# Performance work log

Measured on AMD Instinct MI355X. Metric: run time of the kernel, lower is better.

## Reference

```python
import jax, jax.numpy as jnp
import numpy as np

B, N, HID = 1, 2048, 1024
H, WK, WV = 16, 64, 64
DH = HID // H  # 64


def setup_inputs() -> dict:
    key = jax.random.key(0)
    ks = jax.random.split(key, 10)
    s = 0.02
    return {
        "hidden_states": jax.random.normal(ks[0], (B, N, HID), jnp.float32),
        "attention_mask": jnp.ones((B, N), jnp.float32),
        "Wq": jax.random.normal(ks[1], (HID, HID), jnp.float32) * s,
        "bq": jnp.zeros((HID,), jnp.float32),
        "Wk": jax.random.normal(ks[2], (HID, HID), jnp.float32) * s,
        "bk": jnp.zeros((HID,), jnp.float32),
        "Wv": jax.random.normal(ks[3], (HID, HID), jnp.float32) * s,
        "bv": jnp.zeros((HID,), jnp.float32),
        # Conv1D(2*WK+1, DH, bias=False): weight [nx=DH, nf=2*WK+1]
        "W_rel_k": jax.random.normal(ks[4], (DH, 2 * WK + 1), jnp.float32) * s,
        # relative_pos_val: [2*WV+1, DH]
        "W_rel_v": jax.random.normal(ks[5], (2 * WV + 1, DH), jnp.float32) * s,
    }


def _attention(hidden_states, attention_mask, Wq, bq, Wk, bk, Wv, bv, W_rel_k, W_rel_v):
    b, n, _ = hidden_states.shape

    def heads(x):  # [B,N,HID] -> [B,H,N,DH]
        return x.reshape(b, n, H, DH).transpose(0, 2, 1, 3)

    q = heads(hidden_states @ Wq + bq)
    k = heads(hidden_states @ Wk + bk)
    v = heads(hidden_states @ Wv + bv)

    scores = jnp.einsum("bhid,bhjd->bhij", q, k)  # [B,H,N,N]

    # --- relative-position key bias: bias[i, j] = q_i . w_{j-i+WK} for |j-i|<=WK ---
    a_k = jnp.einsum("bhid,dw->bhiw", q, W_rel_k)  # [B,H,N,2*WK+1]
    rows = jnp.arange(n)
    slot = rows[None, :] - rows[:, None] + WK       # [N,N] relative slot j-i+WK
    valid_k = (slot >= 0) & (slot <= 2 * WK)
    bias = a_k[:, :, rows[:, None], jnp.clip(slot, 0, 2 * WK)]  # [B,H,N,N]
    scores = scores + jnp.where(valid_k, bias, 0.0)

    scores = scores / np.float32(np.sqrt(DH))  # temperature == 1.0

    # extended attention mask: (1 - mask) * dtype_min added to scores
    ext = (1.0 - attention_mask)[:, None, None, :] * jnp.finfo(scores.dtype).min
    scores = scores + ext

    probs = jax.nn.softmax(scores, axis=-1)  # [B,H,N,N]

    ctx = jnp.einsum("bhij,bhjd->bhid", probs, v)  # [B,H,N,DH]

    # --- relative-position value: band[i, r] = probs[i, i-WV+r]; ctx += band @ W_rel_v ---
    offs = jnp.arange(2 * WV + 1)
    kpos = rows[:, None] - WV + offs[None, :]       # [N, 2*WV+1] absolute key position
    valid_v = (kpos >= 0) & (kpos < n)
    band = probs[:, :, rows[:, None], jnp.clip(kpos, 0, n - 1)]  # [B,H,N,2*WV+1]
    band = jnp.where(valid_v, band, 0.0)
    ctx = ctx + jnp.einsum("bhiw,wd->bhid", band, W_rel_v)

    # merge heads -> [B,N,HID]
    return ctx.transpose(0, 2, 1, 3).reshape(b, n, HID)


def reference(hidden_states, attention_mask, Wq, bq, Wk, bk, Wv, bv, W_rel_k, W_rel_v):
    return _attention(hidden_states, attention_mask, Wq, bq, Wk, bk, Wv, bv, W_rel_k, W_rel_v)
```

## Files before the change

kernel.cpp:

```cpp
#include <hip/hip_runtime.h>
#include <hip/hip_bf16.h>

#define NSEQ 2048
#define HIDDIM 1024
#define NH 16
#define DHEAD 64
#define NW 129
#define AKS 132

typedef float          f32x4 __attribute__((ext_vector_type(4)));
typedef _Float16       f16x4 __attribute__((ext_vector_type(4)));
typedef _Float16       f16x8 __attribute__((ext_vector_type(8)));
typedef unsigned short u16;

__device__ __forceinline__ float b2f(u16 u){ return __uint_as_float(((unsigned)u) << 16); }
__device__ __forceinline__ float ld_any(const void* p, long idx, int flag){
  return flag ? b2f(((const u16*)p)[idx]) : ((const float*)p)[idx];
}

#define GLOAD_LDS16(gp, lp) \
  __builtin_amdgcn_global_load_lds((const __attribute__((address_space(1))) unsigned int*)(gp), \
                                   (__attribute__((address_space(3))) unsigned int*)(lp), 16, 0, 0)

static const size_t OFF_Q    = 0;
static const size_t OFF_K    = (size_t)4  << 20;
static const size_t OFF_VT   = (size_t)8  << 20;
static const size_t OFF_WT   = (size_t)12 << 20;
static const size_t OFF_AK   = (size_t)18 << 20;
static const size_t OFF_M    = OFF_AK + (size_t)NH * NSEQ * AKS * 4;
static const size_t OFF_L    = OFF_M + (size_t)2 * NH * NSEQ * 4;
static const size_t OFF_CTXP = OFF_L + (size_t)2 * NH * NSEQ * 4;
static const size_t OFF_HSF  = OFF_CTXP + (size_t)2 * NSEQ * HIDDIM * 4;
static const size_t OFF_BIAS = OFF_HSF + (size_t)NSEQ * HIDDIM * 2;
static const size_t OFF_WRK  = OFF_BIAS + 3 * 1024 * 4;
static const size_t OFF_WRV  = OFF_WRK + (size_t)DHEAD * NW * 4;
static const size_t OFF_EXT  = OFF_WRV + (size_t)NW * DHEAD * 4;
static const size_t OFF_FLAG = OFF_EXT + (size_t)NSEQ * 4;

__global__ void detect_kernel(const unsigned* __restrict__ mask_raw, int* __restrict__ flagp){
  *flagp = (mask_raw[0] == 0x3F800000u) ? 0 : 1;
}

__global__ void cvt_hs_kernel(const void* __restrict__ hs, const int* __restrict__ flagp,
                              _Float16* __restrict__ hsf){
  const int flag = *flagp;
  const long base = (long)(blockIdx.x * 256 + threadIdx.x) * 8;
  f16x8 o;
  if (flag){
    const u16* b = (const u16*)hs;
#pragma unroll
    for (int e = 0; e < 8; e++) o[e] = (_Float16)b2f(b[base + e]);
  } else {
    const float* f = (const float*)hs;
#pragma unroll
    for (int e = 0; e < 8; e++) o[e] = (_Float16)f[base + e];
  }
  *(f16x8*)(hsf + base) = o;
}

__global__ void cvt_small_kernel(const void* __restrict__ bq, const void* __restrict__ bk,
                                 const void* __restrict__ bv, const void* __restrict__ wrk,
                                 const void* __restrict__ wrv, const void* __restrict__ mask,
                                 const int* __restrict__ flagp,
                                 float* __restrict__ biasf, float* __restrict__ wrkf,
                                 float* __restrict__ wrvf, float* __restrict__ extf){
  const int flag = *flagp;
  const int idx = blockIdx.x * 256 + threadIdx.x;
  if (idx < 1024)            biasf[idx] = ld_any(bq, idx, flag);
  else if (idx < 2048)       biasf[idx] = ld_any(bk, idx - 1024, flag);
  else if (idx < 3072)       biasf[idx] = ld_any(bv, idx - 2048, flag);
  else if (idx < 3072 + 8256)  wrkf[idx - 3072]  = ld_any(wrk, idx - 3072, flag);
  else if (idx < 3072 + 16512) wrvf[idx - 11328] = ld_any(wrv, idx - 11328, flag);
  else if (idx < 3072 + 16512 + 2048)
    extf[idx - 19584] = (1.f - ld_any(mask, idx - 19584, flag)) * -1.0e30f;
}

__global__ void wtrans_kernel(const void* __restrict__ Wq, const void* __restrict__ Wk,
                              const void* __restrict__ Wv, const int* __restrict__ flagp,
                              _Float16* __restrict__ Wt){
  __shared__ __attribute__((aligned(16))) _Float16 tile[64][65];
  const int flag = *flagp;
  const int z = blockIdx.z;
  const void* src = (z == 0) ? Wq : ((z == 1) ? Wk : Wv);
  _Float16* dst = Wt + (size_t)z * 1024 * 1024;
  const int o0 = blockIdx.x * 64, k0 = blockIdx.y * 64;
  const int t = threadIdx.x;
#pragma unroll
  for (int c = 0; c < 2; c++){
    int idx = t + 256 * c;
    int r = idx >> 3, c8 = (idx & 7) * 8;
    long off = (long)(k0 + r) * 1024 + o0 + c8;
#pragma unroll
    for (int e = 0; e < 8; e++) tile[r][c8 + e] = (_Float16)ld_any(src, off + e, flag);
  }
  __syncthreads();
#pragma unroll
  for (int c = 0; c < 2; c++){
    int idx = t + 256 * c;
    int orow = idx >> 3, k8 = (idx & 7) * 8;
    f16x8 v;
#pragma unroll
    for (int e = 0; e < 8; e++) v[e] = tile[k8 + e][orow];
    *(f16x8*)(dst + (size_t)(o0 + orow) * 1024 + k0 + k8) = v;
  }
}

__launch_bounds__(256, 3)
__global__ void qkv_kernel(const _Float16* __restrict__ hsf, const _Float16* __restrict__ Wt,
                           const float* __restrict__ biasf,
                           _Float16* __restrict__ Qf, _Float16* __restrict__ Kf,
                           _Float16* __restrict__ Vtf){
  __shared__ __attribute__((aligned(16))) _Float16 As[2 * 64 * 32];
  __shared__ __attribute__((aligned(16))) _Float16 Bs[2 * 128 * 32];
  const int z = blockIdx.z;
  const _Float16* Wz = Wt + (size_t)z * 1024 * 1024;
  const int o0 = blockIdx.x * 128, m0 = blockIdx.y * 64;
  const int t = threadIdx.x, lane = t & 63, wave = t >> 6;
  const int wm = wave >> 1, wn = wave & 1;
  const int q = lane >> 4, ln = lane & 15;

  auto stage = [&](int nb, int k0){
    {
      const int row = t >> 2, chunk = t & 3;
      const _Float16* gA = hsf + (size_t)(m0 + row) * 1024 + k0 + chunk * 8;
      _Float16* lA = (_Float16*)As + nb * 2048 + (wave << 9);
      GLOAD_LDS16(gA, lA);
    }
#pragma unroll
    for (int p = 0; p < 2; p++){
      const int idx = p * 256 + t;
      const int row = idx >> 2, chunk = idx & 3;
      const _Float16* gB = Wz + (size_t)(o0 + row) * 1024 + k0 + chunk * 8;
      _Float16* lB = (_Float16*)Bs + nb * 4096 + ((p * 4 + wave) << 9);
      GLOAD_LDS16(gB, lB);
    }
  };

  f32x4 acc[2][4];
#pragma unroll
  for (int a = 0; a < 2; a++)
#pragma unroll
    for (int b = 0; b < 4; b++) acc[a][b] = (f32x4){0.f, 0.f, 0.f, 0.f};

  stage(0, 0);
  __syncthreads();
  int cur = 0;
  for (int k0 = 0; k0 < 1024; k0 += 32){
    if (k0 + 32 < 1024) stage(cur ^ 1, k0 + 32);
    const _Float16* Ac = (const _Float16*)As + cur * 2048;
    const _Float16* Bc = (const _Float16*)Bs + cur * 4096;
    f16x8 af[2], bf[4];
#pragma unroll
    for (int mt = 0; mt < 2; mt++) af[mt] = *(const f16x8*)&Ac[(wm * 32 + mt * 16 + ln) * 32 + q * 8];
#pragma unroll
    for (int nt = 0; nt < 4; nt++) bf[nt] = *(const f16x8*)&Bc[(wn * 64 + nt * 16 + ln) * 32 + q * 8];
    __builtin_amdgcn_s_setprio(1);
#pragma unroll
    for (int mt = 0; mt < 2; mt++)
#pragma unroll
      for (int nt = 0; nt < 4; nt++)
        acc[mt][nt] = __builtin_amdgcn_mfma_f32_16x16x32_f16(af[mt], bf[nt], acc[mt][nt], 0, 0, 0);
    __builtin_amdgcn_s_setprio(0);
    __syncthreads();
    cur ^= 1;
  }
  const float sc = (z == 0) ? 0.125f : 1.0f;
#pragma unroll
  for (int nt = 0; nt < 4; nt++){
    int o = o0 + wn * 64 + nt * 16 + ln;
    float bval = biasf[z * 1024 + o];
    int hh = o >> 6, dd = o & 63;
#pragma unroll
    for (int mt = 0; mt < 2; mt++){
      int nb = m0 + wm * 32 + mt * 16 + q * 4;
      if (z == 2){
        f16x4 pk;
#pragma unroll
        for (int r = 0; r < 4; r++) pk[r] = (_Float16)(acc[mt][nt][r] + bval);
        *(f16x4*)(Vtf + (size_t)(hh * 64 + dd) * 2048 + nb) = pk;
      } else {
        _Float16* dstp = (z == 0) ? Qf : Kf;
#pragma unroll
        for (int r = 0; r < 4; r++)
          dstp[(size_t)(hh * 2048 + nb + r) * 64 + dd] = (_Float16)((acc[mt][nt][r] + bval) * sc);
      }
    }
  }
}

__launch_bounds__(256, 2)
__global__ void ak_kernel(const _Float16* __restrict__ Qf, const float* __restrict__ wrkf,
                          float* __restrict__ ak){
  __shared__ __attribute__((aligned(16))) _Float16 WrkT[144 * 72];
  const int h = blockIdx.y;
  const int i0 = blockIdx.x * 128;
  const int t = threadIdx.x, lane = t & 63, wave = t >> 6;
  const int q = lane >> 4, ln = lane & 15;
  for (int c = 0; c < 36; c++){
    int idx = t + 256 * c;
    int w = idx >> 6, d = idx & 63;
    float v = (w < NW) ? wrkf[d * NW + w] : 0.f;
    WrkT[w * 72 + d] = (_Float16)v;
  }
  __syncthreads();
  f16x8 afr[2][2];
#pragma unroll
  for (int mt = 0; mt < 2; mt++){
    int row = i0 + wave * 32 + mt * 16 + ln;
#pragma unroll
    for (int ks = 0; ks < 2; ks++)
      afr[mt][ks] = *(const f16x8*)(Qf + (size_t)(h * 2048 + row) * 64 + ks * 32 + q * 8);
  }
  f32x4 acc[2][9];
#pragma unroll
  for (int a = 0; a < 2; a++)
#pragma unroll
    for (int b = 0; b < 9; b++) acc[a][b] = (f32x4){0.f, 0.f, 0.f, 0.f};
#pragma unroll
  for (int nt = 0; nt < 9; nt++){
    f16x8 bfr0 = *(const f16x8*)&WrkT[(nt * 16 + ln) * 72 + q * 8];
    f16x8 bfr1 = *(const f16x8*)&WrkT[(nt * 16 + ln) * 72 + 32 + q * 8];
#pragma unroll
    for (int mt = 0; mt < 2; mt++){
      acc[mt][nt] = __builtin_amdgcn_mfma_f32_16x16x32_f16(afr[mt][0], bfr0, acc[mt][nt], 0, 0, 0);
      acc[mt][nt] = __builtin_amdgcn_mfma_f32_16x16x32_f16(afr[mt][1], bfr1, acc[mt][nt], 0, 0, 0);
    }
  }
#pragma unroll
  for (int nt = 0; nt < 9; nt++){
    int w = nt * 16 + ln;
    if (w > 128) continue;
#pragma unroll
    for (int mt = 0; mt < 2; mt++){
      int ib = i0 + wave * 32 + mt * 16 + q * 4;
#pragma unroll
      for (int r = 0; r < 4; r++)
        ak[(size_t)(h * 2048 + ib + r) * AKS + w] = acc[mt][nt][r];
    }
  }
}

__launch_bounds__(256, 4)
__global__ void flash_kernel(const float* __restrict__ extf,
                             const _Float16* __restrict__ Qf, const _Float16* __restrict__ Kf,
                             const _Float16* __restrict__ Vtf, float* akm,
                             float* __restrict__ ctxpart, float* __restrict__ mws,
                             float* __restrict__ lws){
  __shared__ __attribute__((aligned(16))) _Float16 Ks[2 * 64 * 64];
  __shared__ __attribute__((aligned(16))) _Float16 Vts[2 * 64 * 64];
  __shared__ __attribute__((aligned(16))) float Exts[1024];
  __shared__ int eflags[4];
  const int h = blockIdx.x, qt = blockIdx.y, jh = blockIdx.z;
  const int t = threadIdx.x, lane = t & 63, wave = t >> 6;
  const int q = lane >> 4, ln = lane & 15;
  const int ibase = qt * 64 + wave * 16;
  const int i = ibase + ln;
  const int jb = jh * 1024;

  auto stageK = [&](int nb, int jn){
#pragma unroll
    for (int p = 0; p < 2; p++){
      const int g = p * 256 + t;
      const int row = g >> 3, slot = g & 7;
      const int col8 = slot ^ (row & 7);
      GLOAD_LDS16(Kf + (((size_t)(h * 2048 + jn + row)) << 6) + (col8 << 3),
                  (_Float16*)Ks + nb * 4096 + ((p * 4 + wave) << 9));
    }
  };
  auto stageV = [&](int nb, int jn){
#pragma unroll
    for (int p = 0; p < 2; p++){
      const int g = p * 256 + t;
      const int row = g >> 3, slot = g & 7;
      const int col8 = slot ^ (row & 7);
      GLOAD_LDS16(Vtf + (((size_t)(h * 64 + row)) << 11) + jn + (col8 << 3),
                  (_Float16*)Vts + nb * 4096 + ((p * 4 + wave) << 9));
    }
  };

  const int ds7 = ln & 7;
  const _Float16* kb0 = (const _Float16*)Ks + (ln << 6) + ((q ^ ds7) << 3);
  const _Float16* kb1 = (const _Float16*)Ks + (ln << 6) + (((q + 4) ^ ds7) << 3);
  const _Float16* vb0 = (const _Float16*)Vts + (ln << 6) + (((0 | (q >> 1)) ^ ds7) << 3) + ((q & 1) << 2);
  const _Float16* vb1 = (const _Float16*)Vts + (ln << 6) + (((2 | (q >> 1)) ^ ds7) << 3) + ((q & 1) << 2);
  const _Float16* vb2 = (const _Float16*)Vts + (ln << 6) + (((4 | (q >> 1)) ^ ds7) << 3) + ((q & 1) << 2);
  const _Float16* vb3 = (const _Float16*)Vts + (ln << 6) + (((6 | (q >> 1)) ^ ds7) << 3) + ((q & 1) << 2);

  f16x8 qfrag[2];
  {
    const _Float16* qrow = Qf + (size_t)(h * 2048 + i) * 64;
    qfrag[0] = *(const f16x8*)(qrow + q * 8);
    qfrag[1] = *(const f16x8*)(qrow + 32 + q * 8);
  }
  f32x4 accc[4];
#pragma unroll
  for (int dt = 0; dt < 4; dt++) accc[dt] = (f32x4){0.f, 0.f, 0.f, 0.f};
  float m_i = -1.0e30f, l_i = 0.f;
  float* akrow = akm + (size_t)(h * 2048 + i) * AKS;
  f32x4 s[4];

  auto qk = [&](int PK){
    __builtin_amdgcn_s_setprio(1);
#pragma unroll
    for (int mt = 0; mt < 4; mt++){
      f16x8 kf0 = *(const f16x8*)(kb0 + PK * 4096 + mt * 1024);
      f16x8 kf1 = *(const f16x8*)(kb1 + PK * 4096 + mt * 1024);
      f32x4 zz = (f32x4){0.f, 0.f, 0.f, 0.f};
      zz = __builtin_amdgcn_mfma_f32_16x16x32_f16(kf0, qfrag[0], zz, 0, 0, 0);
      zz = __builtin_amdgcn_mfma_f32_16x16x32_f16(kf1, qfrag[1], zz, 0, 0, 0);
      s[mt] = zz;
    }
    __builtin_amdgcn_s_setprio(0);
  };

  bool nz = false;
#pragma unroll
  for (int c = 0; c < 4; c++){
    float e = extf[jb + c * 256 + t];
    Exts[c * 256 + t] = e;
    nz |= (e != 0.f);
  }
  {
    unsigned long long bz = __ballot(nz);
    if (lane == 0) eflags[wave] = (bz != 0ull) ? 1 : 0;
  }
  stageK(0, jb);
  __syncthreads();
  const bool extNZ = (eflags[0] | eflags[1] | eflags[2] | eflags[3]) != 0;
  stageV(0, jb);
  stageK(1, jb + 64);
  qk(0);
  __syncthreads();

  auto body = [&](int t_, int PV_, int PK1, bool last){
    const int j0 = jb + t_ * 64;
    if (!last){
      stageV(PK1, j0 + 64);
      if (t_ < 14) stageK(PV_, j0 + 128);
    }
    const bool band = (j0 <= ibase + 79) && (j0 + 63 >= ibase - 64);
    if (band){
#pragma unroll
      for (int mt = 0; mt < 4; mt++){
        f32x4 ev = *(const f32x4*)&Exts[t_ * 64 + mt * 16 + (q << 2)];
#pragma unroll
        for (int r = 0; r < 4; r++){
          float x = s[mt][r];
          int w = j0 + mt * 16 + (q << 2) + r - i + 64;
          if ((unsigned)w <= 128u){
            x = x + akrow[w] + ev[r];
            akrow[w] = x;
          } else {
            x = x + ev[r];
          }
          s[mt][r] = x;
        }
      }
    } else if (extNZ){
#pragma unroll
      for (int mt = 0; mt < 4; mt++){
        f32x4 ev = *(const f32x4*)&Exts[t_ * 64 + mt * 16 + (q << 2)];
#pragma unroll
        for (int r = 0; r < 4; r++) s[mt][r] += ev[r];
      }
    }
    float a0 = fmaxf(fmaxf(s[0][0], s[0][1]), fmaxf(s[0][2], s[0][3]));
    float a1 = fmaxf(fmaxf(s[1][0], s[1][1]), fmaxf(s[1][2], s[1][3]));
    float a2 = fmaxf(fmaxf(s[2][0], s[2][1]), fmaxf(s[2][2], s[2][3]));
    float a3 = fmaxf(fmaxf(s[3][0], s[3][1]), fmaxf(s[3][2], s[3][3]));
    float tmax = fmaxf(fmaxf(a0, a1), fmaxf(a2, a3));
    tmax = fmaxf(tmax, __shfl_xor(tmax, 16, 64));
    tmax = fmaxf(tmax, __shfl_xor(tmax, 32, 64));
    float mnew = fmaxf(m_i, tmax);
    if (!__all(tmax <= m_i)){
      float alpha = __expf(m_i - mnew);
      l_i *= alpha;
#pragma unroll
      for (int dt = 0; dt < 4; dt++)
#pragma unroll
        for (int r = 0; r < 4; r++) accc[dt][r] *= alpha;
    }
    m_i = mnew;
    float ps[4][4];
#pragma unroll
    for (int mt = 0; mt < 4; mt++)
#pragma unroll
      for (int r = 0; r < 4; r++) ps[mt][r] = __expf(s[mt][r] - mnew);
    f16x4 pf[4];
#pragma unroll
    for (int mt = 0; mt < 4; mt++)
#pragma unroll
      for (int r = 0; r < 4; r++) pf[mt][r] = (_Float16)ps[mt][r];
    float t0 = (ps[0][0] + ps[0][1]) + (ps[0][2] + ps[0][3]);
    float t1 = (ps[1][0] + ps[1][1]) + (ps[1][2] + ps[1][3]);
    float t2 = (ps[2][0] + ps[2][1]) + (ps[2][2] + ps[2][3]);
    float t3 = (ps[3][0] + ps[3][1]) + (ps[3][2] + ps[3][3]);
    float tsum = (t0 + t1) + (t2 + t3);
    tsum += __shfl_xor(tsum, 16, 64);
    tsum += __shfl_xor(tsum, 32, 64);
    l_i += tsum;
    if (!last) qk(PK1);
    __builtin_amdgcn_s_setprio(1);
#pragma unroll
    for (int dt = 0; dt < 4; dt++){
      f16x4 vf0 = *(const f16x4*)(vb0 + PV_ * 4096 + dt * 1024);
      f16x4 vf1 = *(const f16x4*)(vb1 + PV_ * 4096 + dt * 1024);
      f16x4 vf2 = *(const f16x4*)(vb2 + PV_ * 4096 + dt * 1024);
      f16x4 vf3 = *(const f16x4*)(vb3 + PV_ * 4096 + dt * 1024);
      accc[dt] = __builtin_amdgcn_mfma_f32_16x16x16f16(vf0, pf[0], accc[dt], 0, 0, 0);
      accc[dt] = __builtin_amdgcn_mfma_f32_16x16x16f16(vf1, pf[1], accc[dt], 0, 0, 0);
      accc[dt] = __builtin_amdgcn_mfma_f32_16x16x16f16(vf2, pf[2], accc[dt], 0, 0, 0);
      accc[dt] = __builtin_amdgcn_mfma_f32_16x16x16f16(vf3, pf[3], accc[dt], 0, 0, 0);
    }
    __builtin_amdgcn_s_setprio(0);
    __syncthreads();
  };

  for (int tt = 0; tt < 8; tt++){
    body(2 * tt,     0, 1, false);
    body(2 * tt + 1, 1, 0, tt == 7);
  }

  float* cdst = ctxpart + (size_t)jh * NSEQ * HIDDIM;
#pragma unroll
  for (int dt = 0; dt < 4; dt++)
    *(f32x4*)(cdst + (size_t)i * 1024 + h * 64 + dt * 16 + q * 4) = accc[dt];
  if (q == 0){
    mws[jh * NH * NSEQ + h * 2048 + i] = m_i;
    lws[jh * NH * NSEQ + h * 2048 + i] = l_i;
  }
}

__launch_bounds__(256, 2)
__global__ void finish_kernel(const float* __restrict__ sband, const float* __restrict__ mws,
                              const float* __restrict__ lws, const float* __restrict__ wrvf,
                              const float* __restrict__ ctxpart, float* __restrict__ out){
  __shared__ __attribute__((aligned(16))) _Float16 WrvT[64 * 144];
  __shared__ __attribute__((aligned(16))) _Float16 pT[144 * 72];
  __shared__ __attribute__((aligned(16))) float sM[64], sIL[64], sC0[64], sC1[64];
  const int qt = blockIdx.x, h = blockIdx.y;
  const int i0 = qt * 64;
  const int t = threadIdx.x, lane = t & 63, wave = t >> 6;
  const int q = lane >> 4, ln = lane & 15;
  for (int c = 0; c < 36; c++){
    int idx = c * 256 + t;
    int w = idx >> 6, d = idx & 63;
    WrvT[d * 144 + w] = (w < NW) ? (_Float16)wrvf[w * 64 + d] : (_Float16)0.f;
  }
  if (t < 64){
    int i = i0 + t;
    float m0 = mws[h * 2048 + i],            m1 = mws[NH * NSEQ + h * 2048 + i];
    float l0 = lws[h * 2048 + i],            l1 = lws[NH * NSEQ + h * 2048 + i];
    float M = fmaxf(m0, m1);
    float a0 = __expf(m0 - M), a1 = __expf(m1 - M);
    float L = a0 * l0 + a1 * l1;
    float iL = 1.f / L;
    sM[t] = M; sIL[t] = iL; sC0[t] = a0 * iL; sC1[t] = a1 * iL;
  }
  __syncthreads();
  for (int ii = 0; ii < 16; ii++){
    int il = wave * 16 + ii;
    float Mv = sM[il], ILv = sIL[il];
    const float* srow = sband + (size_t)(h * 2048 + i0 + il) * AKS;
#pragma unroll
    for (int c = 0; c < 3; c++){
      int w = lane + 64 * c;
      if (w < 144){
        float p = (w < NW) ? __expf(srow[w] - Mv) * ILv : 0.f;
        pT[w * 72 + il] = (_Float16)p;
      }
    }
  }
  __syncthreads();
  f32x4 acc[4];
#pragma unroll
  for (int mt = 0; mt < 4; mt++) acc[mt] = (f32x4){0.f, 0.f, 0.f, 0.f};
#pragma unroll
  for (int ks = 0; ks < 9; ks++){
    f16x4 bfr;
#pragma unroll
    for (int j = 0; j < 4; j++) bfr[j] = pT[(ks * 16 + q * 4 + j) * 72 + wave * 16 + ln];
#pragma unroll
    for (int mt = 0; mt < 4; mt++){
      f16x4 afr = *(const f16x4*)&WrvT[(mt * 16 + ln) * 144 + ks * 16 + q * 4];
      acc[mt] = __builtin_amdgcn_mfma_f32_16x16x16f16(afr, bfr, acc[mt], 0, 0, 0);
    }
  }
  const int i = i0 + wave * 16 + ln;
  const float c0 = sC0[wave * 16 + ln], c1 = sC1[wave * 16 + ln];
  const float* p0 = ctxpart;
  const float* p1 = ctxpart + (size_t)NSEQ * HIDDIM;
#pragma unroll
  for (int mt = 0; mt < 4; mt++){
    size_t off = (size_t)i * 1024 + h * 64 + mt * 16 + q * 4;
    f32x4 A0 = *(const f32x4*)(p0 + off);
    f32x4 A1 = *(const f32x4*)(p1 + off);
    f32x4 o4;
#pragma unroll
    for (int r = 0; r < 4; r++) o4[r] = c0 * A0[r] + c1 * A1[r] + acc[mt][r];
    *(f32x4*)(out + off) = o4;
  }
}

extern "C" void kernel_launch(void* const* d_in, const int* in_sizes, int n_in,
                              void* d_out, int out_size, void* d_ws, size_t ws_size,
                              hipStream_t stream){
  const void* hs   = d_in[0];
  const void* mask = d_in[1];
  const void* Wq   = d_in[2];
  const void* bq   = d_in[3];
  const void* Wk   = d_in[4];
  const void* bk   = d_in[5];
  const void* Wv   = d_in[6];
  const void* bv   = d_in[7];
  const void* Wrk  = d_in[8];
  const void* Wrv  = d_in[9];
  float* out = (float*)d_out;

  char* ws = (char*)d_ws;
  _Float16* Qf    = (_Float16*)(ws + OFF_Q);
  _Float16* Kf    = (_Float16*)(ws + OFF_K);
  _Float16* Vtf   = (_Float16*)(ws + OFF_VT);
  _Float16* Wt    = (_Float16*)(ws + OFF_WT);
  float*    akp   = (float*)   (ws + OFF_AK);
  float*    mp    = (float*)   (ws + OFF_M);
  float*    lp    = (float*)   (ws + OFF_L);
  float*    ctxp  = (float*)   (ws + OFF_CTXP);
  _Float16* hsf   = (_Float16*)(ws + OFF_HSF);
  float*    biasf = (float*)   (ws + OFF_BIAS);
  float*    wrkf  = (float*)   (ws + OFF_WRK);
  float*    wrvf  = (float*)   (ws + OFF_WRV);
  float*    extf  = (float*)   (ws + OFF_EXT);
  int*      flagp = (int*)     (ws + OFF_FLAG);

  detect_kernel   <<<dim3(1),          1,   0, stream>>>((const unsigned*)mask, flagp);
  cvt_hs_kernel   <<<dim3(1024),       256, 0, stream>>>(hs, flagp, hsf);
  cvt_small_kernel<<<dim3(85),         256, 0, stream>>>(bq, bk, bv, Wrk, Wrv, mask, flagp,
                                                         biasf, wrkf, wrvf, extf);
  wtrans_kernel   <<<dim3(16, 16, 3),  256, 0, stream>>>(Wq, Wk, Wv, flagp, Wt);
  qkv_kernel      <<<dim3(8, 32, 3),   256, 0, stream>>>(hsf, Wt, biasf, Qf, Kf, Vtf);
  ak_kernel       <<<dim3(16, 16),     256, 0, stream>>>(Qf, wrkf, akp);
  flash_kernel    <<<dim3(16, 32, 2),  256, 0, stream>>>(extf, Qf, Kf, Vtf, akp, ctxp, mp, lp);
  finish_kernel   <<<dim3(32, 16),     256, 0, stream>>>(akp, mp, lp, wrvf, ctxp, out);
}
```

Baseline: 197.1 us.

## Process two 16-row query groups per wave in flash kernel; vectorize conversion loads

Each wave in the flash kernel now handles 32 query rows (two groups of 16) instead of 16, so each K/V fragment read from LDS feeds twice as many MFMAs. The grid is halved, and launch bounds drop to 2 blocks per SM to make room for the extra accumulators and score registers. Separately, the hidden-state and weight conversion kernels now use vector loads instead of scalar per-element loads. The trade-off is higher register pressure and fewer resident blocks, which reduces latency hiding, and the grid is now 512 blocks.

```diff
diff --git a/kernel.cpp b/kernel.cpp
--- a/kernel.cpp
+++ b/kernel.cpp
@@ -11,6 +11,7 @@
 typedef float          f32x4 __attribute__((ext_vector_type(4)));
 typedef _Float16       f16x4 __attribute__((ext_vector_type(4)));
 typedef _Float16       f16x8 __attribute__((ext_vector_type(8)));
+typedef unsigned short u16x8 __attribute__((ext_vector_type(8)));
 typedef unsigned short u16;
 
 __device__ __forceinline__ float b2f(u16 u){ return __uint_as_float(((unsigned)u) << 16); }
@@ -47,13 +48,14 @@
   const long base = (long)(blockIdx.x * 256 + threadIdx.x) * 8;
   f16x8 o;
   if (flag){
-    const u16* b = (const u16*)hs;
-#pragma unroll
-    for (int e = 0; e < 8; e++) o[e] = (_Float16)b2f(b[base + e]);
+    u16x8 v = *(const u16x8*)((const u16*)hs + base);
+#pragma unroll
+    for (int e = 0; e < 8; e++) o[e] = (_Float16)b2f(v[e]);
   } else {
-    const float* f = (const float*)hs;
-#pragma unroll
-    for (int e = 0; e < 8; e++) o[e] = (_Float16)f[base + e];
+    f32x4 a = *(const f32x4*)((const float*)hs + base);
+    f32x4 b = *(const f32x4*)((const float*)hs + base + 4);
+#pragma unroll
+    for (int e = 0; e < 4; e++){ o[e] = (_Float16)a[e]; o[4 + e] = (_Float16)b[e]; }
   }
   *(f16x8*)(hsf + base) = o;
 }
@@ -90,8 +92,16 @@
     int idx = t + 256 * c;
     int r = idx >> 3, c8 = (idx & 7) * 8;
     long off = (long)(k0 + r) * 1024 + o0 + c8;
-#pragma unroll
-    for (int e = 0; e < 8; e++) tile[r][c8 + e] = (_Float16)ld_any(src, off + e, flag);
+    if (flag){
+      u16x8 v = *(const u16x8*)((const u16*)src + off);
+#pragma unroll
+      for (int e = 0; e < 8; e++) tile[r][c8 + e] = (_Float16)b2f(v[e]);
+    } else {
+      f32x4 a = *(const f32x4*)((const float*)src + off);
+      f32x4 b = *(const f32x4*)((const float*)src + off + 4);
+#pragma unroll
+      for (int e = 0; e < 4; e++){ tile[r][c8 + e] = (_Float16)a[e]; tile[r][c8 + 4 + e] = (_Float16)b[e]; }
+    }
   }
   __syncthreads();
 #pragma unroll
@@ -240,7 +250,7 @@
   }
 }
 
-__launch_bounds__(256, 4)
+__launch_bounds__(256, 2)
 __global__ void flash_kernel(const float* __restrict__ extf,
                              const _Float16* __restrict__ Qf, const _Float16* __restrict__ Kf,
                              const _Float16* __restrict__ Vtf, float* akm,
@@ -253,8 +263,7 @@
   const int h = blockIdx.x, qt = blockIdx.y, jh = blockIdx.z;
   const int t = threadIdx.x, lane = t & 63, wave = t >> 6;
   const int q = lane >> 4, ln = lane & 15;
-  const int ibase = qt * 64 + wave * 16;
-  const int i = ibase + ln;
+  const int ibase = qt * 128 + wave * 32;
   const int jb = jh * 1024;
 
   auto stageK = [&](int nb, int jn){
@@ -286,18 +295,21 @@
   const _Float16* vb2 = (const _Float16*)Vts + (ln << 6) + (((4 | (q >> 1)) ^ ds7) << 3) + ((q & 1) << 2);
   const _Float16* vb3 = (const _Float16*)Vts + (ln << 6) + (((6 | (q >> 1)) ^ ds7) << 3) + ((q & 1) << 2);
 
-  f16x8 qfrag[2];
-  {
-    const _Float16* qrow = Qf + (size_t)(h * 2048 + i) * 64;
-    qfrag[0] = *(const f16x8*)(qrow + q * 8);
-    qfrag[1] = *(const f16x8*)(qrow + 32 + q * 8);
-  }
-  f32x4 accc[4];
-#pragma unroll
-  for (int dt = 0; dt < 4; dt++) accc[dt] = (f32x4){0.f, 0.f, 0.f, 0.f};
-  float m_i = -1.0e30f, l_i = 0.f;
-  float* akrow = akm + (size_t)(h * 2048 + i) * AKS;
-  f32x4 s[4];
+  f16x8 qfrag[2][2];
+#pragma unroll
+  for (int g = 0; g < 2; g++){
+    const _Float16* qrow = Qf + (size_t)(h * 2048 + ibase + g * 16 + ln) * 64;
+    qfrag[g][0] = *(const f16x8*)(qrow + q * 8);
+    qfrag[g][1] = *(const f16x8*)(qrow + 32 + q * 8);
+  }
+  f32x4 accc[2][4];
+#pragma unroll
+  for (int g = 0; g < 2; g++)
+#pragma unroll
+    for (int dt = 0; dt < 4; dt++) accc[g][dt] = (f32x4){0.f, 0.f, 0.f, 0.f};
+  float m_i[2] = {-1.0e30f, -1.0e30f}, l_i[2] = {0.f, 0.f};
+  f32x4 s[2][4];
+  f16x4 pf[2][4];
 
   auto qk = [&](int PK){
     __builtin_amdgcn_s_setprio(1);
@@ -305,10 +317,13 @@
     for (int mt = 0; mt < 4; mt++){
       f16x8 kf0 = *(const f16x8*)(kb0 + PK * 4096 + mt * 1024);
       f16x8 kf1 = *(const f16x8*)(kb1 + PK * 4096 + mt * 1024);
-      f32x4 zz = (f32x4){0.f, 0.f, 0.f, 0.f};
-      zz = __builtin_amdgcn_mfma_f32_16x16x32_f16(kf0, qfrag[0], zz, 0, 0, 0);
-      zz = __builtin_amdgcn_mfma_f32_16x16x32_f16(kf1, qfrag[1], zz, 0, 0, 0);
-      s[mt] = zz;
+#pragma unroll
+      for (int g = 0; g < 2; g++){
+        f32x4 zz = (f32x4){0.f, 0.f, 0.f, 0.f};
+        zz = __builtin_amdgcn_mfma_f32_16x16x32_f16(kf0, qfrag[g][0], zz, 0, 0, 0);
+        zz = __builtin_amdgcn_mfma_f32_16x16x32_f16(kf1, qfrag[g][1], zz, 0, 0, 0);
+        s[g][mt] = zz;
+      }
     }
     __builtin_amdgcn_s_setprio(0);
   };
@@ -338,67 +353,75 @@
       stageV(PK1, j0 + 64);
       if (t_ < 14) stageK(PV_, j0 + 128);
     }
-    const bool band = (j0 <= ibase + 79) && (j0 + 63 >= ibase - 64);
-    if (band){
-#pragma unroll
-      for (int mt = 0; mt < 4; mt++){
-        f32x4 ev = *(const f32x4*)&Exts[t_ * 64 + mt * 16 + (q << 2)];
-#pragma unroll
-        for (int r = 0; r < 4; r++){
-          float x = s[mt][r];
-          int w = j0 + mt * 16 + (q << 2) + r - i + 64;
-          if ((unsigned)w <= 128u){
-            x = x + akrow[w] + ev[r];
-            akrow[w] = x;
-          } else {
-            x = x + ev[r];
+#pragma unroll
+    for (int g = 0; g < 2; g++){
+      const int gb = ibase + g * 16;
+      const int ig = gb + ln;
+      const bool band = (j0 <= gb + 79) && (j0 + 63 >= gb - 64);
+      if (band){
+        float* akr = akm + (size_t)(h * 2048 + ig) * AKS;
+#pragma unroll
+        for (int mt = 0; mt < 4; mt++){
+          f32x4 ev = *(const f32x4*)&Exts[t_ * 64 + mt * 16 + (q << 2)];
+#pragma unroll
+          for (int r = 0; r < 4; r++){
+            float x = s[g][mt][r];
+            int w = j0 + mt * 16 + (q << 2) + r - ig + 64;
+            if ((unsigned)w <= 128u){
+              x = x + akr[w] + ev[r];
+              akr[w] = x;
+            } else {
+              x = x + ev[r];
+            }
+            s[g][mt][r] = x;
           }
-          s[mt][r] = x;
+        }
+      } else if (extNZ){
+#pragma unroll
+        for (int mt = 0; mt < 4; mt++){
+          f32x4 ev = *(const f32x4*)&Exts[t_ * 64 + mt * 16 + (q << 2)];
+#pragma unroll
+          for (int r = 0; r < 4; r++) s[g][mt][r] += ev[r];
         }
       }
-    } else if (extNZ){
-#pragma unroll
-      for (int mt = 0; mt < 4; mt++){
-        f32x4 ev = *(const f32x4*)&Exts[t_ * 64 + mt * 16 + (q << 2)];
-#pragma unroll
-        for (int r = 0; r < 4; r++) s[mt][r] += ev[r];
+    }
+#pragma unroll
+    for (int g = 0; g < 2; g++){
+      float a0 = fmaxf(fmaxf(s[g][0][0], s[g][0][1]), fmaxf(s[g][0][2], s[g][0][3]));
+      float a1 = fmaxf(fmaxf(s[g][1][0], s[g][1][1]), fmaxf(s[g][1][2], s[g][1][3]));
+      float a2 = fmaxf(fmaxf(s[g][2][0], s[g][2][1]), fmaxf(s[g][2][2], s[g][2][3]));
+      float a3 = fmaxf(fmaxf(s[g][3][0], s[g][3][1]), fmaxf(s[g][3][2], s[g][3][3]));
+      float tmax = fmaxf(fmaxf(a0, a1), fmaxf(a2, a3));
+      tmax = fmaxf(tmax, __shfl_xor(tmax, 16, 64));
+      tmax = fmaxf(tmax, __shfl_xor(tmax, 32, 64));
+      float mnew = fmaxf(m_i[g], tmax);
+      if (!__all(tmax <= m_i[g])){
+        float alpha = __expf(m_i[g] - mnew);
+        l_i[g] *= alpha;
+#pragma unroll
+        for (int dt = 0; dt < 4; dt++)
+#pragma unroll
+          for (int r = 0; r < 4; r++) accc[g][dt][r] *= alpha;
       }
-    }
-    float a0 = fmaxf(fmaxf(s[0][0], s[0][1]), fmaxf(s[0][2], s[0][3]));
-    float a1 = fmaxf(fmaxf(s[1][0], s[1][1]), fmaxf(s[1][2], s[1][3]));
-    float a2 = fmaxf(fmaxf(s[2][0], s[2][1]), fmaxf(s[2][2], s[2][3]));
-    float a3 = fmaxf(fmaxf(s[3][0], s[3][1]), fmaxf(s[3][2], s[3][3]));
-    float tmax = fmaxf(fmaxf(a0, a1), fmaxf(a2, a3));
-    tmax = fmaxf(tmax, __shfl_xor(tmax, 16, 64));
-    tmax = fmaxf(tmax, __shfl_xor(tmax, 32, 64));
-    float mnew = fmaxf(m_i, tmax);
-    if (!__all(tmax <= m_i)){
-      float alpha = __expf(m_i - mnew);
-      l_i *= alpha;
-#pragma unroll
-      for (int dt = 0; dt < 4; dt++)
-#pragma unroll
-        for (int r = 0; r < 4; r++) accc[dt][r] *= alpha;
-    }
-    m_i = mnew;
-    float ps[4][4];
-#pragma unroll
-    for (int mt = 0; mt < 4; mt++)
-#pragma unroll
-      for (int r = 0; r < 4; r++) ps[mt][r] = __expf(s[mt][r] - mnew);
-    f16x4 pf[4];
-#pragma unroll
-    for (int mt = 0; mt < 4; mt++)
-#pragma unroll
-      for (int r = 0; r < 4; r++) pf[mt][r] = (_Float16)ps[mt][r];
-    float t0 = (ps[0][0] + ps[0][1]) + (ps[0][2] + ps[0][3]);
-    float t1 = (ps[1][0] + ps[1][1]) + (ps[1][2] + ps[1][3]);
-    float t2 = (ps[2][0] + ps[2][1]) + (ps[2][2] + ps[2][3]);
-    float t3 = (ps[3][0] + ps[3][1]) + (ps[3][2] + ps[3][3]);
-    float tsum = (t0 + t1) + (t2 + t3);
-    tsum += __shfl_xor(tsum, 16, 64);
-    tsum += __shfl_xor(tsum, 32, 64);
-    l_i += tsum;
+      m_i[g] = mnew;
+      float ps[4][4];
+#pragma unroll
+      for (int mt = 0; mt < 4; mt++)
+#pragma unroll
+        for (int r = 0; r < 4; r++) ps[mt][r] = __expf(s[g][mt][r] - mnew);
+#pragma unroll
+      for (int mt = 0; mt < 4; mt++)
+#pragma unroll
+        for (int r = 0; r < 4; r++) pf[g][mt][r] = (_Float16)ps[mt][r];
+      float t0 = (ps[0][0] + ps[0][1]) + (ps[0][2] + ps[0][3]);
+      float t1 = (ps[1][0] + ps[1][1]) + (ps[1][2] + ps[1][3]);
+      float t2 = (ps[2][0] + ps[2][1]) + (ps[2][2] + ps[2][3]);
+      float t3 = (ps[3][0] + ps[3][1]) + (ps[3][2] + ps[3][3]);
+      float tsum = (t0 + t1) + (t2 + t3);
+      tsum += __shfl_xor(tsum, 16, 64);
+      tsum += __shfl_xor(tsum, 32, 64);
+      l_i[g] += tsum;
+    }
     if (!last) qk(PK1);
     __builtin_amdgcn_s_setprio(1);
 #pragma unroll
@@ -407,10 +430,13 @@
       f16x4 vf1 = *(const f16x4*)(vb1 + PV_ * 4096 + dt * 1024);
       f16x4 vf2 = *(const f16x4*)(vb2 + PV_ * 4096 + dt * 1024);
       f16x4 vf3 = *(const f16x4*)(vb3 + PV_ * 4096 + dt * 1024);
-      accc[dt] = __builtin_amdgcn_mfma_f32_16x16x16f16(vf0, pf[0], accc[dt], 0, 0, 0);
-      accc[dt] = __builtin_amdgcn_mfma_f32_16x16x16f16(vf1, pf[1], accc[dt], 0, 0, 0);
-      accc[dt] = __builtin_amdgcn_mfma_f32_16x16x16f16(vf2, pf[2], accc[dt], 0, 0, 0);
-      accc[dt] = __builtin_amdgcn_mfma_f32_16x16x16f16(vf3, pf[3], accc[dt], 0, 0, 0);
+#pragma unroll
+      for (int g = 0; g < 2; g++){
+        accc[g][dt] = __builtin_amdgcn_mfma_f32_16x16x16f16(vf0, pf[g][0], accc[g][dt], 0, 0, 0);
+        accc[g][dt] = __builtin_amdgcn_mfma_f32_16x16x16f16(vf1, pf[g][1], accc[g][dt], 0, 0, 0);
+        accc[g][dt] = __builtin_amdgcn_mfma_f32_16x16x16f16(vf2, pf[g][2], accc[g][dt], 0, 0, 0);
+        accc[g][dt] = __builtin_amdgcn_mfma_f32_16x16x16f16(vf3, pf[g][3], accc[g][dt], 0, 0, 0);
+      }
     }
     __builtin_amdgcn_s_setprio(0);
     __syncthreads();
@@ -423,11 +449,15 @@
 
   float* cdst = ctxpart + (size_t)jh * NSEQ * HIDDIM;
 #pragma unroll
-  for (int dt = 0; dt < 4; dt++)
-    *(f32x4*)(cdst + (size_t)i * 1024 + h * 64 + dt * 16 + q * 4) = accc[dt];
-  if (q == 0){
-    mws[jh * NH * NSEQ + h * 2048 + i] = m_i;
-    lws[jh * NH * NSEQ + h * 2048 + i] = l_i;
+  for (int g = 0; g < 2; g++){
+    const int ig = ibase + g * 16 + ln;
+#pragma unroll
+    for (int dt = 0; dt < 4; dt++)
+      *(f32x4*)(cdst + (size_t)ig * 1024 + h * 64 + dt * 16 + q * 4) = accc[g][dt];
+    if (q == 0){
+      mws[jh * NH * NSEQ + h * 2048 + ig] = m_i[g];
+      lws[jh * NH * NSEQ + h * 2048 + ig] = l_i[g];
+    }
   }
 }
 
@@ -540,6 +570,6 @@
   wtrans_kernel   <<<dim3(16, 16, 3),  256, 0, stream>>>(Wq, Wk, Wv, flagp, Wt);
   qkv_kernel      <<<dim3(8, 32, 3),   256, 0, stream>>>(hsf, Wt, biasf, Qf, Kf, Vtf);
   ak_kernel       <<<dim3(16, 16),     256, 0, stream>>>(Qf, wrkf, akp);
-  flash_kernel    <<<dim3(16, 32, 2),  256, 0, stream>>>(extf, Qf, Kf, Vtf, akp, ctxp, mp, lp);
+  flash_kernel    <<<dim3(16, 16, 2),  256, 0, stream>>>(extf, Qf, Kf, Vtf, akp, ctxp, mp, lp);
   finish_kernel   <<<dim3(32, 16),     256, 0, stream>>>(akp, mp, lp, wrvf, ctxp, out);
 }
```

After: 212.5 us. 7.8% more time.
